# Kernel tuning notes

Hardware: AMD Instinct MI355X
Metric: run time of the kernel (lower is better)

Reference implementation:

```python
import math
import jax, jax.numpy as jnp
import numpy as np

NUM_BUCKETS = 32
MAX_DISTANCE = 128
NUM_HEADS = 16


def _relative_position_bucket_bidirectional(relative_position):
    # encoder (is_decoder=False): split buckets for positive/negative, then log-spaced
    nb = NUM_BUCKETS // 2  # 16
    buckets = (relative_position > 0).astype(jnp.int32) * nb
    rp = jnp.abs(relative_position)
    max_exact = nb // 2  # 8
    is_small = rp < max_exact
    rp_safe = jnp.maximum(rp, 1)  # avoid log(0); masked out by is_small anyway
    large = max_exact + (
        jnp.log(rp_safe.astype(jnp.float32) / max_exact)
        / math.log(MAX_DISTANCE / max_exact)
        * (nb - max_exact)
    ).astype(jnp.int32)
    large = jnp.minimum(large, nb - 1)
    return buckets + jnp.where(is_small, rp, large)


def compute_bias(rel_bias, tgt_len, src_len):
    ctx = jnp.arange(tgt_len)[:, None]
    mem = jnp.arange(src_len)[None, :]
    buckets = _relative_position_bucket_bidirectional(mem - ctx)  # [T,S]
    values = rel_bias[buckets]            # [T,S,H]
    return jnp.transpose(values, (2, 0, 1))[None]  # [1,H,T,S]


def setup_inputs() -> dict:
    key = jax.random.key(0)
    ks = jax.random.split(key, 7)
    B, S, D = 4, 2048, 1024
    s = 1.0 / math.sqrt(D)
    return {
        "query_states": jax.random.normal(ks[0], (B, S, D), jnp.float32),
        "key_value_states": jax.random.normal(ks[1], (B, S, D), jnp.float32),
        "wq": jax.random.normal(ks[2], (D, D), jnp.float32) * s,
        "wk": jax.random.normal(ks[3], (D, D), jnp.float32) * s,
        "wv": jax.random.normal(ks[4], (D, D), jnp.float32) * s,
        "wo": jax.random.normal(ks[5], (D, D), jnp.float32) * s,
        "rel_bias": jax.random.normal(ks[6], (NUM_BUCKETS, NUM_HEADS), jnp.float32),
    }


def reference(query_states, key_value_states, wq, wk, wv, wo, rel_bias):
    B, T, D = query_states.shape
    S = key_value_states.shape[1]
    H = NUM_HEADS
    dh = D // H

    def shape(x, L):
        return jnp.transpose(x.reshape(B, L, H, dh), (0, 2, 1, 3))  # [B,H,L,dh]

    q = shape(query_states @ wq, T)
    k = shape(key_value_states @ wk, S)
    v = shape(key_value_states @ wv, S)

    bias = compute_bias(rel_bias, T, S)                      # [1,H,T,S]
    scores = jnp.einsum("bhtd,bhsd->bhts", q, k) + bias      # no 1/sqrt(d) scaling (T5)
    weights = jax.nn.softmax(scores, axis=-1)
    attn = jnp.einsum("bhts,bhsd->bhtd", weights, v)
    attn = jnp.transpose(attn, (0, 2, 1, 3)).reshape(B, T, D)
    return attn @ wo
```

## Files before the change

### kernel.cpp

```cpp
#include <hip/hip_runtime.h>
#include <hip/hip_bf16.h>
#include <math.h>

typedef __bf16 bf16;
typedef __attribute__((ext_vector_type(8))) __bf16 bf16x8;
typedef __attribute__((ext_vector_type(4))) __bf16 bf16x4;
typedef __attribute__((ext_vector_type(4))) float f32x4;
typedef __attribute__((ext_vector_type(16))) float f32x16;
typedef __attribute__((ext_vector_type(4), aligned(4))) float f32x4u;

#define B_  4
#define S_  2048
#define D_  1024
#define H_  16
#define DH_ 64
#define M_  (B_ * S_)
#define LOG2E 1.44269504088896f

static __device__ __forceinline__ f32x4 mfma16(bf16x8 a, bf16x8 b, f32x4 c) {
  return __builtin_amdgcn_mfma_f32_16x16x32_bf16(a, b, c, 0, 0, 0);
}
static __device__ __forceinline__ f32x16 mfma32(bf16x8 a, bf16x8 b, f32x16 c) {
  return __builtin_amdgcn_mfma_f32_32x32x16_bf16(a, b, c, 0, 0, 0);
}

static __device__ __forceinline__ void gld_lds16(const bf16* g, bf16* l) {
  __builtin_amdgcn_global_load_lds(
      (const __attribute__((address_space(1))) void*)g,
      (__attribute__((address_space(3))) void*)l, 16, 0, 0);
}

static __device__ __forceinline__ unsigned pkbf(float a, float b) {
  union { struct { __bf16 lo, hi; } s; unsigned u; } x;
  x.s.lo = (bf16)a; x.s.hi = (bf16)b;
  return x.u;
}

__global__ __launch_bounds__(256)
void cast2_kernel(const float* __restrict__ a, const float* __restrict__ bsrc,
                  bf16* __restrict__ oa, bf16* __restrict__ ob) {
  const int blk = blockIdx.x;
  const float* in = (blk < 8192) ? a : bsrc;
  bf16* out = (blk < 8192) ? oa : ob;
  size_t i = ((size_t)(blk & 8191) * 256 + threadIdx.x) * 4;
  float4 v = *(const float4*)(in + i);
  bf16x4 o = {(bf16)v.x, (bf16)v.y, (bf16)v.z, (bf16)v.w};
  *(bf16x4*)(out + i) = o;
}

__global__ __launch_bounds__(256)
void transpose_cast4_kernel(const float* __restrict__ w0, const float* __restrict__ w1,
                            const float* __restrict__ w2, const float* __restrict__ w3,
                            bf16* __restrict__ o0, bf16* __restrict__ o1,
                            bf16* __restrict__ o2, bf16* __restrict__ o3) {
  __shared__ float tile[32][33];
  const int z = blockIdx.z;
  const float* in = (z == 0) ? w0 : (z == 1) ? w1 : (z == 2) ? w2 : w3;
  bf16* out = (z == 0) ? o0 : (z == 1) ? o1 : (z == 2) ? o2 : o3;
  int n0 = blockIdx.x * 32, k0 = blockIdx.y * 32;
  int tx = threadIdx.x, ty = threadIdx.y;
#pragma unroll
  for (int j = 0; j < 32; j += 8)
    tile[ty + j][tx] = in[(size_t)(k0 + ty + j) * D_ + n0 + tx];
  __syncthreads();
#pragma unroll
  for (int j = 0; j < 32; j += 8)
    out[(size_t)(n0 + ty + j) * D_ + k0 + tx] = (bf16)tile[tx][ty + j];
}

__global__ __launch_bounds__(256)
void bias_table_kernel(const float* __restrict__ rel_bias, float* __restrict__ tab) {
  int i = blockIdx.x * 256 + threadIdx.x;
  int h = i >> 12, dp = i & 4095;
  int rel = dp - 2047;
  int bucket = (rel > 0) ? 16 : 0;
  int rp = rel < 0 ? -rel : rel;
  if (rp < 8) {
    bucket += rp;
  } else {
    int large = 8 + (int)(2.0f * __log2f((float)rp * 0.125f));
    bucket += (large < 15 ? large : 15);
  }
  tab[i] = rel_bias[bucket * H_ + h] * LOG2E - 64.0f;
}

__global__ __launch_bounds__(256)
void proj_gemm_kernel(const bf16* __restrict__ Xq, const bf16* __restrict__ Xkv,
                      const bf16* __restrict__ Wq, const bf16* __restrict__ Wk,
                      const bf16* __restrict__ Wv,
                      bf16* __restrict__ Qb, bf16* __restrict__ Kb, bf16* __restrict__ Vt) {
  const int K = D_;
  __shared__ bf16 As[128][32];
  __shared__ bf16 Bs[128][32];
  const int z = blockIdx.z;
  const bf16* A  = (z == 0) ? Xq : Xkv;
  const bf16* Bt = (z == 0) ? Wq : (z == 1) ? Wk : Wv;
  const int tid = threadIdx.x;
  const int brow = blockIdx.y * 128, bcol = blockIdx.x * 128;
  const int wave = tid >> 6, lane = tid & 63;
  const int wr = (wave >> 1) * 64, wc = (wave & 1) * 64;
  const int lrow = lane & 15, lgrp = lane >> 4;

  f32x4 acc[4][4] = {};

  const bf16* ag = A + (size_t)(brow + (tid >> 2)) * K + (tid & 3) * 8;
  const bf16* bg = Bt + (size_t)(bcol + (tid >> 2)) * K + (tid & 3) * 8;
  const size_t rstep = (size_t)64 * K;
  bf16* al = &As[0][0] + tid * 8;
  bf16* bl = &Bs[0][0] + tid * 8;

  for (int k0 = 0; k0 < K; k0 += 32) {
    __syncthreads();
    gld_lds16(ag + k0, al);
    gld_lds16(ag + k0 + rstep, al + 64 * 32);
    gld_lds16(bg + k0, bl);
    gld_lds16(bg + k0 + rstep, bl + 64 * 32);
    __syncthreads();
    bf16x8 af[4], bfr[4];
#pragma unroll
    for (int i = 0; i < 4; ++i) {
      af[i]  = *(const bf16x8*)&As[wr + i * 16 + lrow][lgrp * 8];
      bfr[i] = *(const bf16x8*)&Bs[wc + i * 16 + lrow][lgrp * 8];
    }
#pragma unroll
    for (int mi = 0; mi < 4; ++mi)
#pragma unroll
      for (int ni = 0; ni < 4; ++ni)
        acc[mi][ni] = mfma16(af[mi], bfr[ni], acc[mi][ni]);
  }

  const float scl = (z == 0) ? LOG2E : 1.0f;
#pragma unroll
  for (int mi = 0; mi < 4; ++mi) {
    const int rowb = brow + wr + mi * 16 + lgrp * 4;
#pragma unroll
    for (int ni = 0; ni < 4; ++ni) {
      const int col = bcol + wc + ni * 16 + lrow;
#pragma unroll
      for (int r = 0; r < 4; ++r) {
        const float v = acc[mi][ni][r] * scl;
        const int m = rowb + r;
        const int bb = m >> 11, s = m & (S_ - 1);
        const int hh = col >> 6, d = col & (DH_ - 1);
        if (z == 0)
          Qb[((size_t)((bb * H_ + hh) * S_ + s)) * DH_ + d] = (bf16)v;
        else if (z == 1)
          Kb[((size_t)((bb * H_ + hh) * S_ + s)) * DH_ + d] = (bf16)v;
        else
          Vt[((size_t)((bb * H_ + hh) * DH_ + d)) * S_ + s] = (bf16)v;
      }
    }
  }
}

__global__ __launch_bounds__(256)
void gemm_out_kernel(const bf16* __restrict__ A, const bf16* __restrict__ Bt,
                     float* __restrict__ Cout) {
  const int K = D_, N = D_;
  __shared__ bf16 As[128][32];
  __shared__ bf16 Bs[128][32];
  const int tid = threadIdx.x;
  const int brow = blockIdx.y * 128, bcol = blockIdx.x * 128;
  const int wave = tid >> 6, lane = tid & 63;
  const int wr = (wave >> 1) * 64, wc = (wave & 1) * 64;
  const int lrow = lane & 15, lgrp = lane >> 4;

  f32x4 acc[4][4] = {};

  const bf16* ag = A + (size_t)(brow + (tid >> 2)) * K + (tid & 3) * 8;
  const bf16* bg = Bt + (size_t)(bcol + (tid >> 2)) * K + (tid & 3) * 8;
  const size_t rstep = (size_t)64 * K;
  bf16* al = &As[0][0] + tid * 8;
  bf16* bl = &Bs[0][0] + tid * 8;

  for (int k0 = 0; k0 < K; k0 += 32) {
    __syncthreads();
    gld_lds16(ag + k0, al);
    gld_lds16(ag + k0 + rstep, al + 64 * 32);
    gld_lds16(bg + k0, bl);
    gld_lds16(bg + k0 + rstep, bl + 64 * 32);
    __syncthreads();
    bf16x8 af[4], bfr[4];
#pragma unroll
    for (int i = 0; i < 4; ++i) {
      af[i]  = *(const bf16x8*)&As[wr + i * 16 + lrow][lgrp * 8];
      bfr[i] = *(const bf16x8*)&Bs[wc + i * 16 + lrow][lgrp * 8];
    }
#pragma unroll
    for (int mi = 0; mi < 4; ++mi)
#pragma unroll
      for (int ni = 0; ni < 4; ++ni)
        acc[mi][ni] = mfma16(af[mi], bfr[ni], acc[mi][ni]);
  }

#pragma unroll
  for (int mi = 0; mi < 4; ++mi) {
    const int rowb = brow + wr + mi * 16 + lgrp * 4;
#pragma unroll
    for (int ni = 0; ni < 4; ++ni) {
      const int col = bcol + wc + ni * 16 + lrow;
#pragma unroll
      for (int r = 0; r < 4; ++r)
        Cout[(size_t)(rowb + r) * N + col] = acc[mi][ni][r];
    }
  }
}

__global__ __launch_bounds__(256, 4)
void attn_kernel(const bf16* __restrict__ Q, const bf16* __restrict__ Kb,
                 const bf16* __restrict__ Vt, const float* __restrict__ tab,
                 bf16* __restrict__ Oa) {
  __shared__ bf16 SB[4][4096];

  const int bid = blockIdx.x;
  const int w = ((bid & 7) << 7) + (bid >> 3);
  const int qt = w & 15, h = (w >> 4) & 15, b = w >> 8;
  const int tid = threadIdx.x;
  const int wave = tid >> 6, lane = tid & 63;
  const int l31 = lane & 31;
  const int hi = lane >> 5;
  const int t = qt * 128 + wave * 32 + l31;

  const bf16* Qp = Q + (size_t)(b * H_ + h) * S_ * DH_;
  const bf16* Kp = Kb + (size_t)(b * H_ + h) * S_ * DH_;
  const bf16* Vp = Vt + (size_t)(b * H_ + h) * DH_ * S_;
  const float* btb = tab + h * 4096 + 2047 - t;

  const int row0 = tid >> 4, row1 = row0 + 16;
  const int colS = (tid & 15) << 4;
  const int col0 = colS ^ ((row0 & 15) << 4);
  const int col1 = colS ^ ((row1 & 15) << 4);
  const bf16* ks0 = Kp + (size_t)(row0 + 32 * (col0 >> 7)) * DH_ + ((col0 & 127) >> 1);
  const bf16* ks1 = Kp + (size_t)(row1 + 32 * (col1 >> 7)) * DH_ + ((col1 & 127) >> 1);
  const bf16* vs0 = Vp + (size_t)(row0 + 32 * (col0 >> 7)) * S_ + ((col0 & 127) >> 1);
  const bf16* vs1 = Vp + (size_t)(row1 + 32 * (col1 >> 7)) * S_ + ((col1 & 127) >> 1);
  bf16* sd = &SB[0][0] + tid * 8;

  const int swz = (l31 & 15) << 4;
  const char* rb = (const char*)&SB[0][0] + l31 * 256;
  const char* ra[4][2];
#pragma unroll
  for (int c = 0; c < 4; ++c)
#pragma unroll
    for (int sub = 0; sub < 2; ++sub)
      ra[c][sub] = rb + ((c * 32 + hi * 16 + sub * 128) ^ swz);

  bf16x8 qf[4];
#pragma unroll
  for (int c = 0; c < 4; ++c)
    qf[c] = *(const bf16x8*)&Qp[(size_t)t * DH_ + c * 16 + hi * 8];

  float l_r = 0.f;
  f32x16 o0 = {}, o1 = {};

  gld_lds16(ks0, sd); gld_lds16(ks1, sd + 2048);
  gld_lds16(vs0, sd + 8192); gld_lds16(vs1, sd + 10240);
  __syncthreads();

#define ATTN_TILE(BUF, S0)                                                        \
  {                                                                               \
    if ((S0) + 64 < S_) {                                                         \
      const int nb = (BUF) ^ 1;                                                   \
      gld_lds16(ks0 + (size_t)((S0) + 64) * DH_, sd + nb * 4096);                 \
      gld_lds16(ks1 + (size_t)((S0) + 64) * DH_, sd + nb * 4096 + 2048);          \
      gld_lds16(vs0 + ((S0) + 64), sd + nb * 4096 + 8192);                        \
      gld_lds16(vs1 + ((S0) + 64), sd + nb * 4096 + 10240);                       \
    }                                                                             \
    f32x16 sc0, sc1;                                                              \
    _Pragma("unroll")                                                             \
    for (int g = 0; g < 4; ++g) {                                                 \
      f32x4u b0 = *(const f32x4u*)(btb + (S0) + 8 * g + 4 * hi);                  \
      f32x4u b1 = *(const f32x4u*)(btb + (S0) + 32 + 8 * g + 4 * hi);             \
      _Pragma("unroll")                                                           \
      for (int v = 0; v < 4; ++v) { sc0[4 * g + v] = b0[v]; sc1[4 * g + v] = b1[v]; } \
    }                                                                             \
    _Pragma("unroll")                                                             \
    for (int c = 0; c < 4; ++c) {                                                 \
      bf16x8 k0 = *(const bf16x8*)(ra[c][0] + (BUF) * 8192);                      \
      bf16x8 k1 = *(const bf16x8*)(ra[c][1] + (BUF) * 8192);                      \
      sc0 = mfma32(k0, qf[c], sc0);                                               \
      sc1 = mfma32(k1, qf[c], sc1);                                               \
    }                                                                             \
    unsigned pw[16];                                                              \
    float q0s = 0.f, q1s = 0.f, q2s = 0.f, q3s = 0.f;                             \
    _Pragma("unroll")                                                             \
    for (int r2 = 0; r2 < 8; ++r2) {                                              \
      float a0 = __builtin_amdgcn_exp2f(sc0[2 * r2]);                             \
      float a1 = __builtin_amdgcn_exp2f(sc0[2 * r2 + 1]);                         \
      float c0 = __builtin_amdgcn_exp2f(sc1[2 * r2]);                             \
      float c1 = __builtin_amdgcn_exp2f(sc1[2 * r2 + 1]);                         \
      q0s += a0; q1s += a1; q2s += c0; q3s += c1;                                 \
      pw[r2] = pkbf(a0, a1);                                                      \
      pw[8 + r2] = pkbf(c0, c1);                                                  \
    }                                                                             \
    l_r += (q0s + q1s) + (q2s + q3s);                                             \
                 \
    unsigned sh[8];                                                               \
    _Pragma("unroll")                                                             \
    for (int g = 0; g < 4; ++g) {                                                 \
      const int base = (g & 1) * 4 + (g >> 1) * 8;                                \
      sh[2 * g]     = __shfl_xor(hi ? pw[base + 0] : pw[base + 2], 32);           \
      sh[2 * g + 1] = __shfl_xor(hi ? pw[base + 1] : pw[base + 3], 32);           \
    }                                                                             \
    _Pragma("unroll")                                                             \
    for (int g = 0; g < 4; ++g) {                                                 \
      const int base = (g & 1) * 4 + (g >> 1) * 8;                                \
      int4 bi = { (int)(hi ? sh[2 * g]     : pw[base + 0]),                       \
                  (int)(hi ? sh[2 * g + 1] : pw[base + 1]),                       \
                  (int)(hi ? pw[base + 2] : sh[2 * g]),                           \
                  (int)(hi ? pw[base + 3] : sh[2 * g + 1]) };                     \
      bf16x8 pb = *(bf16x8*)&bi;                                                  \
      bf16x8 v0 = *(const bf16x8*)(ra[g][0] + 16384 + (BUF) * 8192);              \
      bf16x8 v1 = *(const bf16x8*)(ra[g][1] + 16384 + (BUF) * 8192);              \
      o0 = mfma32(v0, pb, o0);                                                    \
      o1 = mfma32(v1, pb, o1);                                                    \
    }                                                                             \
    __syncthreads();                                                              \
  }

  for (int s0 = 0; s0 < S_; s0 += 128) {
    ATTN_TILE(0, s0)
    ATTN_TILE(1, s0 + 64)
  }
#undef ATTN_TILE

  l_r += __shfl_xor(l_r, 32);
  const float inv = 1.0f / l_r;
  bf16* Ob = Oa + ((size_t)(b * S_ + t)) * D_ + h * DH_;
#pragma unroll
  for (int g = 0; g < 4; ++g) {
    bf16x4 u0 = {(bf16)(o0[4 * g + 0] * inv), (bf16)(o0[4 * g + 1] * inv),
                 (bf16)(o0[4 * g + 2] * inv), (bf16)(o0[4 * g + 3] * inv)};
    *(bf16x4*)&Ob[8 * g + 4 * hi] = u0;
    bf16x4 u1 = {(bf16)(o1[4 * g + 0] * inv), (bf16)(o1[4 * g + 1] * inv),
                 (bf16)(o1[4 * g + 2] * inv), (bf16)(o1[4 * g + 3] * inv)};
    *(bf16x4*)&Ob[32 + 8 * g + 4 * hi] = u1;
  }
}

extern "C" void kernel_launch(void* const* d_in, const int* in_sizes, int n_in,
                              void* d_out, int out_size, void* d_ws, size_t ws_size,
                              hipStream_t stream) {
  const float* Xq   = (const float*)d_in[0];
  const float* Xkv  = (const float*)d_in[1];
  const float* Wq   = (const float*)d_in[2];
  const float* Wk   = (const float*)d_in[3];
  const float* Wv   = (const float*)d_in[4];
  const float* Wo   = (const float*)d_in[5];
  const float* relb = (const float*)d_in[6];
  float* out = (float*)d_out;

  char* ws = (char*)d_ws;
  const size_t SZ_X = (size_t)M_ * D_ * 2;
  const size_t SZ_W = (size_t)D_ * D_ * 2;
  bf16* Xq_b  = (bf16*)(ws);
  bf16* Xkv_b = (bf16*)(ws + SZ_X);
  bf16* Wq_t  = (bf16*)(ws + 2 * SZ_X);
  bf16* Wk_t  = (bf16*)(ws + 2 * SZ_X + SZ_W);
  bf16* Wv_t  = (bf16*)(ws + 2 * SZ_X + 2 * SZ_W);
  bf16* Wo_t  = (bf16*)(ws + 2 * SZ_X + 3 * SZ_W);
  bf16* Qb    = (bf16*)(ws + 2 * SZ_X + 4 * SZ_W);
  bf16* Kbuf  = (bf16*)(ws + 3 * SZ_X + 4 * SZ_W);
  bf16* Vt    = (bf16*)(ws + 4 * SZ_X + 4 * SZ_W);
  bf16* Ab    = (bf16*)(ws + 5 * SZ_X + 4 * SZ_W);
  float* tab  = (float*)(ws + 6 * SZ_X + 4 * SZ_W);

  cast2_kernel<<<16384, 256, 0, stream>>>(Xq, Xkv, Xq_b, Xkv_b);
  transpose_cast4_kernel<<<dim3(32, 32, 4), dim3(32, 8), 0, stream>>>(
      Wq, Wk, Wv, Wo, Wq_t, Wk_t, Wv_t, Wo_t);
  bias_table_kernel<<<256, 256, 0, stream>>>(relb, tab);

  proj_gemm_kernel<<<dim3(8, 64, 3), 256, 0, stream>>>(
      Xq_b, Xkv_b, Wq_t, Wk_t, Wv_t, Qb, Kbuf, Vt);
  attn_kernel<<<1024, 256, 0, stream>>>(Qb, Kbuf, Vt, tab, Ab);
  gemm_out_kernel<<<dim3(8, 64), 256, 0, stream>>>(Ab, Wo_t, out);
}
```

Measured before the change: 242.8 us.

## Use constant bias for far tiles and vectorize V-transpose stores

Attention tiles far from the diagonal (beyond the max relative distance) now initialise scores with the saturated bias constant instead of loading per-element bias from the table, splitting the key loop into far-low, near, and far-high ranges. The V projection epilogue writes four contiguous sequence positions as one packed bf16x4 store instead of four scalar stores. This cuts global bias loads and scattered stores, at the cost of more code from three unrolled loop copies.

```diff
diff --git a/kernel.cpp b/kernel.cpp
--- a/kernel.cpp
+++ b/kernel.cpp
@@ -136,18 +136,23 @@
 #pragma unroll
     for (int ni = 0; ni < 4; ++ni) {
       const int col = bcol + wc + ni * 16 + lrow;
-#pragma unroll
-      for (int r = 0; r < 4; ++r) {
-        const float v = acc[mi][ni][r] * scl;
-        const int m = rowb + r;
-        const int bb = m >> 11, s = m & (S_ - 1);
-        const int hh = col >> 6, d = col & (DH_ - 1);
-        if (z == 0)
-          Qb[((size_t)((bb * H_ + hh) * S_ + s)) * DH_ + d] = (bf16)v;
-        else if (z == 1)
-          Kb[((size_t)((bb * H_ + hh) * S_ + s)) * DH_ + d] = (bf16)v;
-        else
-          Vt[((size_t)((bb * H_ + hh) * DH_ + d)) * S_ + s] = (bf16)v;
+      const int hh = col >> 6, d = col & (DH_ - 1);
+      if (z == 2) {
+        const int bb = rowb >> 11, s = rowb & (S_ - 1);
+        bf16x4 pk = {(bf16)acc[mi][ni][0], (bf16)acc[mi][ni][1],
+                     (bf16)acc[mi][ni][2], (bf16)acc[mi][ni][3]};
+        *(bf16x4*)&Vt[((size_t)((bb * H_ + hh) * DH_ + d)) * S_ + s] = pk;
+      } else {
+#pragma unroll
+        for (int r = 0; r < 4; ++r) {
+          const float v = acc[mi][ni][r] * scl;
+          const int m = rowb + r;
+          const int bb = m >> 11, s = m & (S_ - 1);
+          if (z == 0)
+            Qb[((size_t)((bb * H_ + hh) * S_ + s)) * DH_ + d] = (bf16)v;
+          else
+            Kb[((size_t)((bb * H_ + hh) * S_ + s)) * DH_ + d] = (bf16)v;
+        }
       }
     }
   }
@@ -219,12 +224,15 @@
   const int wave = tid >> 6, lane = tid & 63;
   const int l31 = lane & 31;
   const int hi = lane >> 5;
-  const int t = qt * 128 + wave * 32 + l31;
+  const int q0b = qt * 128;
+  const int t = q0b + wave * 32 + l31;
 
   const bf16* Qp = Q + (size_t)(b * H_ + h) * S_ * DH_;
   const bf16* Kp = Kb + (size_t)(b * H_ + h) * S_ * DH_;
   const bf16* Vp = Vt + (size_t)(b * H_ + h) * DH_ * S_;
   const float* btb = tab + h * 4096 + 2047 - t;
+  const float c_lo = tab[h * 4096];
+  const float c_hi = tab[h * 4096 + 4095];
 
   const int row0 = tid >> 4, row1 = row0 + 16;
   const int colS = (tid & 15) << 4;
@@ -257,22 +265,13 @@
   gld_lds16(vs0, sd + 8192); gld_lds16(vs1, sd + 10240);
   __syncthreads();
 
-#define ATTN_TILE(BUF, S0)                                                        \
-  {                                                                               \
+#define TILE_BODY(BUF, S0)                                                        \
     if ((S0) + 64 < S_) {                                                         \
       const int nb = (BUF) ^ 1;                                                   \
       gld_lds16(ks0 + (size_t)((S0) + 64) * DH_, sd + nb * 4096);                 \
       gld_lds16(ks1 + (size_t)((S0) + 64) * DH_, sd + nb * 4096 + 2048);          \
       gld_lds16(vs0 + ((S0) + 64), sd + nb * 4096 + 8192);                        \
       gld_lds16(vs1 + ((S0) + 64), sd + nb * 4096 + 10240);                       \
-    }                                                                             \
-    f32x16 sc0, sc1;                                                              \
-    _Pragma("unroll")                                                             \
-    for (int g = 0; g < 4; ++g) {                                                 \
-      f32x4u b0 = *(const f32x4u*)(btb + (S0) + 8 * g + 4 * hi);                  \
-      f32x4u b1 = *(const f32x4u*)(btb + (S0) + 32 + 8 * g + 4 * hi);             \
-      _Pragma("unroll")                                                           \
-      for (int v = 0; v < 4; ++v) { sc0[4 * g + v] = b0[v]; sc1[4 * g + v] = b1[v]; } \
     }                                                                             \
     _Pragma("unroll")                                                             \
     for (int c = 0; c < 4; ++c) {                                                 \
@@ -294,7 +293,6 @@
       pw[8 + r2] = pkbf(c0, c1);                                                  \
     }                                                                             \
     l_r += (q0s + q1s) + (q2s + q3s);                                             \
-                 \
     unsigned sh[8];                                                               \
     _Pragma("unroll")                                                             \
     for (int g = 0; g < 4; ++g) {                                                 \
@@ -315,14 +313,47 @@
       o0 = mfma32(v0, pb, o0);                                                    \
       o1 = mfma32(v1, pb, o1);                                                    \
     }                                                                             \
-    __syncthreads();                                                              \
-  }
-
-  for (int s0 = 0; s0 < S_; s0 += 128) {
-    ATTN_TILE(0, s0)
-    ATTN_TILE(1, s0 + 64)
-  }
-#undef ATTN_TILE
+    __syncthreads();
+
+#define ATTN_NEAR(BUF, S0)                                                        \
+  {                                                                               \
+    f32x16 sc0, sc1;                                                              \
+    _Pragma("unroll")                                                             \
+    for (int g = 0; g < 4; ++g) {                                                 \
+      f32x4u b0 = *(const f32x4u*)(btb + (S0) + 8 * g + 4 * hi);                  \
+      f32x4u b1 = *(const f32x4u*)(btb + (S0) + 32 + 8 * g + 4 * hi);             \
+      _Pragma("unroll")                                                           \
+      for (int v = 0; v < 4; ++v) { sc0[4 * g + v] = b0[v]; sc1[4 * g + v] = b1[v]; } \
+    }                                                                             \
+    TILE_BODY(BUF, S0)                                                            \
+  }
+
+#define ATTN_FAR(BUF, S0, CB)                                                     \
+  {                                                                               \
+    f32x16 sc0, sc1;                                                              \
+    _Pragma("unroll")                                                             \
+    for (int v = 0; v < 16; ++v) { sc0[v] = (CB); sc1[v] = (CB); }                \
+    TILE_BODY(BUF, S0)                                                            \
+  }
+
+  const int near_lo = (q0b - 128 > 0) ? q0b - 128 : 0;
+  const int near_hi = (q0b + 256 < S_) ? q0b + 256 : S_;
+
+  for (int s0 = 0; s0 < near_lo; s0 += 128) {
+    ATTN_FAR(0, s0, c_lo)
+    ATTN_FAR(1, s0 + 64, c_lo)
+  }
+  for (int s0 = near_lo; s0 < near_hi; s0 += 128) {
+    ATTN_NEAR(0, s0)
+    ATTN_NEAR(1, s0 + 64)
+  }
+  for (int s0 = near_hi; s0 < S_; s0 += 128) {
+    ATTN_FAR(0, s0, c_hi)
+    ATTN_FAR(1, s0 + 64, c_hi)
+  }
+#undef ATTN_NEAR
+#undef ATTN_FAR
+#undef TILE_BODY
 
   l_r += __shfl_xor(l_r, 32);
   const float inv = 1.0f / l_r;
```

New measurement: 674.6 us. 178% more time.
